# Kernel tuning notes

Hardware: AMD Instinct MI355X
Metric: run time of the kernel (lower is better)

Reference implementation:

```python
import jax, jax.numpy as jnp
import numpy as np

ATT, WEMB, VIEW, ADIM, EMB = 312, 512, 16, 2048, 2048
B = 2048
IN = ATT + WEMB + VIEW * WEMB  # 9016; output_dim defaults to input_dim
EPS = 1e-8  # torch cosine_similarity eps


def setup_inputs() -> dict:
    key = jax.random.key(0)
    ks = jax.random.split(key, 8)
    s = 0.02
    return {
        "x": jax.random.normal(ks[0], (B, IN), dtype=jnp.float32),
        "Wq": s * jax.random.normal(ks[1], (WEMB, ADIM), dtype=jnp.float32),
        "bq": jnp.zeros((ADIM,), jnp.float32),
        "Wk": s * jax.random.normal(ks[2], (WEMB, ADIM), dtype=jnp.float32),
        "bk": jnp.zeros((ADIM,), jnp.float32),
        "Wv": s * jax.random.normal(ks[3], (WEMB, ADIM), dtype=jnp.float32),
        "bv": jnp.zeros((ADIM,), jnp.float32),
        "Wm": s * jax.random.normal(ks[4], (ATT + ADIM, EMB), dtype=jnp.float32),
        "bm": jnp.zeros((EMB,), jnp.float32),
        "Wd1": s * jax.random.normal(ks[5], (EMB, 4096), dtype=jnp.float32),
        "bd1": jnp.zeros((4096,), jnp.float32),
        "Wd2": s * jax.random.normal(ks[6], (4096, IN), dtype=jnp.float32),
        "bd2": jnp.zeros((IN,), jnp.float32),
    }


def reference(x, Wq, bq, Wk, bk, Wv, bv, Wm, bm, Wd1, bd1, Wd2, bd2):
    att_emb = x[:, :ATT]                                   # [B, 312]
    desc_emb = x[:, ATT:ATT + WEMB]                        # [B, 512]
    gpt_emb = x[:, ATT + WEMB:].reshape(x.shape[0], -1, WEMB)  # [B, V, 512]

    # q is the same projected desc for every view (expand before linear)
    q = desc_emb @ Wq + bq                                 # [B, A]
    k = jnp.einsum("bvw,wa->bva", gpt_emb, Wk) + bk        # [B, V, A]
    v = jnp.einsum("bvw,wa->bva", gpt_emb, Wv) + bv        # [B, V, A]

    # cosed score: cosine similarity * L2 distance
    dot = jnp.einsum("bva,ba->bv", k, q)                   # [B, V]
    qn = jnp.maximum(jnp.linalg.norm(q, axis=-1), EPS)     # [B]
    kn = jnp.maximum(jnp.linalg.norm(k, axis=-1), EPS)     # [B, V]
    cs = dot / (qn[:, None] * kn)
    ed = jnp.linalg.norm(q[:, None, :] - k, axis=-1)       # [B, V]
    attn = jax.nn.softmax(cs * ed, axis=-1)                # [B, V]

    # torch.matmul([B,V], [B,V,A]) -> [B,B,A]; .mean(dim=1) averages over the
    # attn-batch axis, i.e. fused[j] = mean_b(attn[b]) @ v[j]. Compute the
    # mathematically identical form without the BxBxA intermediate.
    attn_mean = attn.mean(axis=0)                          # [V]
    fused = jnp.einsum("v,bva->ba", attn_mean, v)          # [B, A]

    z = jax.nn.relu(jnp.concatenate([att_emb, fused], axis=1) @ Wm + bm)  # [B, EMB]
    h = jax.nn.relu(z @ Wd1 + bd1)                          # [B, 4096]
    return h @ Wd2 + bd2                                    # [B, IN]
```

## Files before the change

### kernel.cpp

```cpp
#include <hip/hip_runtime.h>


typedef __bf16 bf16x8 __attribute__((ext_vector_type(8)));
typedef float  f32x4  __attribute__((ext_vector_type(4)));
typedef unsigned short u16;

#define ATT   312
#define WEMB  512
#define VIEW  16
#define ADIM  2048
#define EMB   2048
#define BATCH 2048
#define INDIM 9016
#define KCAT  2360
#define KCATP 2432
#define NOUT  9016
#define NOUTP 9216

__device__ __forceinline__ u16 f2bf(float f) {
  unsigned u = __builtin_bit_cast(unsigned, f);
  u += 0x7FFFu + ((u >> 16) & 1u);
  return (u16)(u >> 16);
}
__device__ __forceinline__ float bf2f(u16 b) {
  unsigned u = (unsigned)b << 16;
  return __builtin_bit_cast(float, u);
}

__device__ __forceinline__ void gl_lds16(const u16* g, u16* l) {
  __builtin_amdgcn_global_load_lds((const __attribute__((address_space(1))) void*)g,
                                   (__attribute__((address_space(3))) void*)l, 16, 0, 0);
}

__global__ void castx_k(const float* __restrict__ x, u16* __restrict__ cc,
                        u16* __restrict__ desc, u16* __restrict__ gpt) {
  const int b = blockIdx.x, t = threadIdx.x;
  const float4* row = (const float4*)(x + (size_t)b * INDIM);
  for (int c = t; c < INDIM / 4; c += 256) {
    float4 v = row[c];
    ushort4 o = make_ushort4(f2bf(v.x), f2bf(v.y), f2bf(v.z), f2bf(v.w));
    if (c < ATT / 4)                 *(ushort4*)&cc[(size_t)b * KCATP + c * 4] = o;
    else if (c < (ATT + WEMB) / 4)   *(ushort4*)&desc[(size_t)b * WEMB + (c - ATT / 4) * 4] = o;
    else                             *(ushort4*)&gpt[(size_t)b * (VIEW * WEMB) + (c - (ATT + WEMB) / 4) * 4] = o;
  }
  if (t < (KCATP - KCAT) / 4) {
    *(ushort4*)&cc[(size_t)b * KCATP + KCAT + t * 4] = make_ushort4(0, 0, 0, 0);
  }
}

struct TcDesc { const float* src; u16* dst; int K, N, Kp, Np, ntx, base; };
struct TcArgs { TcDesc d[6]; };

__global__ void transcast6_k(TcArgs A) {
  __shared__ float tile[64][65];
  int mi = 0;
  const int bid = blockIdx.x;
#pragma unroll
  for (int i = 1; i < 6; ++i) if (bid >= A.d[i].base) mi = i;
  const TcDesc& D = A.d[mi];
  const int local = bid - D.base;
  const int n0 = (local % D.ntx) * 64, k0 = (local / D.ntx) * 64;
  const int t = threadIdx.x;
  const int tr = t >> 4, tc4 = (t & 15) * 4;
#pragma unroll
  for (int i = 0; i < 4; ++i) {
    const int k = k0 + tr + i * 16;
    float v0 = 0.f, v1 = 0.f, v2 = 0.f, v3 = 0.f;
    if (k < D.K) {
      const int n = n0 + tc4;
      const float* p = D.src + (size_t)k * D.N + n;
      if (n + 3 < D.N) { float4 v = *(const float4*)p; v0 = v.x; v1 = v.y; v2 = v.z; v3 = v.w; }
      else {
        if (n + 0 < D.N) v0 = p[0];
        if (n + 1 < D.N) v1 = p[1];
        if (n + 2 < D.N) v2 = p[2];
        if (n + 3 < D.N) v3 = p[3];
      }
    }
    tile[tr + i * 16][tc4 + 0] = v0;
    tile[tr + i * 16][tc4 + 1] = v1;
    tile[tr + i * 16][tc4 + 2] = v2;
    tile[tr + i * 16][tc4 + 3] = v3;
  }
  __syncthreads();
#pragma unroll
  for (int i = 0; i < 4; ++i) {
    const int rn = tr + i * 16;
    const int n = n0 + rn;
    const int kk = k0 + tc4;
    if (n < D.Np && kk < D.Kp) {
      const bool nv = (n < D.N);
      ushort4 o = make_ushort4(f2bf(nv ? tile[tc4 + 0][rn] : 0.f),
                               f2bf(nv ? tile[tc4 + 1][rn] : 0.f),
                               f2bf(nv ? tile[tc4 + 2][rn] : 0.f),
                               f2bf(nv ? tile[tc4 + 3][rn] : 0.f));
      *(ushort4*)&D.dst[(size_t)n * D.Kp + kk] = o;
    }
  }
}

__device__ __forceinline__ void stage_half(const u16* __restrict__ src, int ld,
                                           u16* dst, int wave, int lane) {
#pragma unroll
  for (int j = 0; j < 2; ++j) {
    const int s = wave * 2 + j;
    const int r = ((s >> 1) << 4) + (lane >> 2);
    const int c = ((s & 1) << 5) +
                  (((lane & 3) << 3) ^ (((lane >> 5) & 1) << 4));
    gl_lds16(src + (long)r * ld + c, dst + s * 512 + (lane << 3));
  }
}

#define BAR   __builtin_amdgcn_s_barrier()
#define LGKM0 asm volatile("s_waitcnt lgkmcnt(0)" ::: "memory")
#define VM6   asm volatile("s_waitcnt vmcnt(6)" ::: "memory")
#define VM4   asm volatile("s_waitcnt vmcnt(4)" ::: "memory")
#define VM0   asm volatile("s_waitcnt vmcnt(0)" ::: "memory")

#define RDA(bufo, lo, hi) do { _Pragma("unroll") for (int mf = (lo); mf <= (hi); ++mf) \
  _Pragma("unroll") for (int kk = 0; kk < 2; ++kk) \
    a[mf][kk] = *(const bf16x8*)&lds[(bufo) + aoff0 + (mf * 2 + kk) * 512]; } while (0)
#define RDB(bufo, lo, hi) do { _Pragma("unroll") for (int nf = (lo); nf <= (hi); ++nf) \
  _Pragma("unroll") for (int kk = 0; kk < 2; ++kk) \
    b[nf][kk] = *(const bf16x8*)&lds[(bufo) + boff0 + nf * 1024 + kk * 512]; } while (0)
#define QUAD(qm, qn) do { __builtin_amdgcn_s_setprio(1); \
  _Pragma("unroll") for (int m4 = 0; m4 < 4; ++m4) \
  _Pragma("unroll") for (int n2 = 0; n2 < 2; ++n2) \
  _Pragma("unroll") for (int kk = 0; kk < 2; ++kk) \
    acc[(qm) * 4 + m4][(qn) * 2 + n2] = __builtin_amdgcn_mfma_f32_16x16x32_bf16( \
        a[(qm) * 4 + m4][kk], b[(qn) * 2 + n2][kk], acc[(qm) * 4 + m4][(qn) * 2 + n2], 0, 0, 0); \
  __builtin_amdgcn_s_setprio(0); } while (0)

template <int MODE>
__global__ __launch_bounds__(512, 2)
void gemm256(const u16* __restrict__ A, const u16* __restrict__ BT,
             const float* __restrict__ bias, int K, int Nreal,
             float* __restrict__ dstF, u16* __restrict__ dstH,
             float* __restrict__ PF, int ldc,
             const float* __restrict__ qbuf, float* __restrict__ dotb,
             float* __restrict__ kn2b, int mt, int nt, int fastm) {
  __shared__ alignas(16) u16 lds[65536];
  int tm, tn, ksl = 0, kloc = K;
  long koff = 0;
  if (MODE == 5) {
    if ((int)blockIdx.x < 256) {
      const int w = ((blockIdx.x & 7) << 5) + (blockIdx.x >> 3);
      tm = w & 7; tn = w >> 3;
    } else {
      const int b2 = blockIdx.x - 256;
      const int w = ((b2 & 7) << 5) + (b2 >> 3);
      const int tile = w >> 3; ksl = w & 7;
      tm = tile & 7; tn = 32 + (tile >> 3);
      kloc = 512; koff = (long)ksl * 512;
    }
  } else if (MODE == 6) {
    const int w = ((blockIdx.x & 7) << 5) + (blockIdx.x >> 3);
    ksl = w & 1;
    const int tile = w >> 1;
    tm = tile & 7; tn = tile >> 3;
    kloc = K >> 1; koff = (long)ksl * kloc;
  } else {
    const int nwg = mt * nt;
    const int xcd = blockIdx.x & 7, idx = blockIdx.x >> 3;
    const int qq = nwg >> 3, rr = nwg & 7;
    const int wg = (xcd < rr ? xcd * (qq + 1) : rr * (qq + 1) + (xcd - rr) * qq) + idx;
    if (fastm) { tm = wg % mt; tn = wg / mt; } else { tn = wg % nt; tm = wg / nt; }
  }

  const int tid = threadIdx.x;
  const int wave = tid >> 6, lane = tid & 63;
  const long m0 = (long)tm * 256, n0 = (long)tn * 256;
  const int wm = wave >> 2, wn = wave & 3;
  const u16* Ab = A + m0 * K + koff;
  const u16* Bb = BT + n0 * K + koff;

  f32x4 acc[8][4] = {};
  bf16x8 a[8][2], b[4][2];
  const int LP = (lane & 15) * 32 + ((((lane >> 4) << 3)) ^ (((lane >> 3) & 1) << 4));
  const int aoff0 = wm * 8192 + LP;
  const int boff0 = 16384 + (wn >> 1) * 8192 + (wn & 1) * 4096 + LP;
  const int NT = kloc >> 6;

  stage_half(Ab,                K, &lds[0],     wave, lane);
  stage_half(Ab + 128 * K,      K, &lds[8192],  wave, lane);
  stage_half(Bb,                K, &lds[16384], wave, lane);
  stage_half(Bb + 128 * K,      K, &lds[24576], wave, lane);
  stage_half(Ab + 64,           K, &lds[32768], wave, lane);
  stage_half(Ab + 128 * K + 64, K, &lds[40960], wave, lane);
  stage_half(Bb + 64,           K, &lds[49152], wave, lane);
  VM6; BAR;

  const int iters = NT >> 1;
  for (int i = 0; i < iters; ++i) {
    const int t0 = 2 * i;
    const bool nl = (i < iters - 1);
    RDA(0, 0, 3); RDB(0, 0, 1);
    stage_half(Bb + 128 * K + (t0 + 1) * 64, K, &lds[57344], wave, lane);
    BAR; LGKM0; QUAD(0, 0); BAR;
    RDA(0, 4, 7);
    BAR; LGKM0; QUAD(1, 0); BAR;
    RDB(0, 2, 3);
    if (nl) stage_half(Ab + (t0 + 2) * 64, K, &lds[0], wave, lane);
    BAR; LGKM0; QUAD(0, 1); BAR;
    if (nl) stage_half(Ab + 128 * K + (t0 + 2) * 64, K, &lds[8192], wave, lane);
    BAR; QUAD(1, 1);
    if (nl) { VM4; } else { VM0; }
    BAR;
    RDA(32768, 0, 3); RDB(32768, 0, 1);
    if (nl) stage_half(Bb + (t0 + 2) * 64, K, &lds[16384], wave, lane);
    BAR; LGKM0; QUAD(0, 0); BAR;
    RDA(32768, 4, 7);
    if (nl) stage_half(Bb + 128 * K + (t0 + 2) * 64, K, &lds[24576], wave, lane);
    BAR; LGKM0; QUAD(1, 0); BAR;
    RDB(32768, 2, 3);
    if (nl) stage_half(Ab + (t0 + 3) * 64, K, &lds[32768], wave, lane);
    BAR; LGKM0; QUAD(0, 1); BAR;
    if (nl) {
      stage_half(Ab + 128 * K + (t0 + 3) * 64, K, &lds[40960], wave, lane);
      stage_half(Bb + (t0 + 3) * 64, K, &lds[49152], wave, lane);
    }
    BAR; QUAD(1, 1);
    if (nl) VM6;
    BAR;
  }

  const int lr = lane >> 4, lc = lane & 15;
  if (MODE == 2) {
#pragma unroll
    for (int mf = 0; mf < 8; ++mf) {
#pragma unroll
      for (int r = 0; r < 4; ++r) {
        const long grow = m0 + wm * 128 + mf * 16 + lr * 4 + r;
        const long bb = grow >> 4;
        float ds = 0.f, ks2 = 0.f;
#pragma unroll
        for (int nf = 0; nf < 4; ++nf) {
          const long col = n0 + wn * 64 + nf * 16 + lc;
          float kv = acc[mf][nf][r] + bias[col];
          ds += kv * qbuf[bb * ADIM + col];
          ks2 += kv * kv;
        }
#pragma unroll
        for (int m = 1; m < 16; m <<= 1) {
          ds += __shfl_xor(ds, m, 64);
          ks2 += __shfl_xor(ks2, m, 64);
        }
        if (lc == 0) {
          atomicAdd(&dotb[grow], ds);
          atomicAdd(&kn2b[grow], ks2);
        }
      }
    }
  } else if (MODE == 5) {
    if (ksl == 0) {
#pragma unroll
      for (int mf = 0; mf < 8; ++mf) {
#pragma unroll
        for (int nf = 0; nf < 4; ++nf) {
          const long col = n0 + wn * 64 + nf * 16 + lc;
          if (col < Nreal) {
            const float bv_ = bias[col];
#pragma unroll
            for (int r = 0; r < 4; ++r) {
              const long row = m0 + wm * 128 + mf * 16 + lr * 4 + r;
              dstF[row * (long)ldc + col] = acc[mf][nf][r] + bv_;
            }
          }
        }
      }
    } else {
      float* pt = PF + (long)(ksl - 1) * BATCH * 1024;
#pragma unroll
      for (int mf = 0; mf < 8; ++mf) {
#pragma unroll
        for (int nf = 0; nf < 4; ++nf) {
          const long col = n0 + wn * 64 + nf * 16 + lc;
#pragma unroll
          for (int r = 0; r < 4; ++r) {
            const long row = m0 + wm * 128 + mf * 16 + lr * 4 + r;
            pt[row * 1024 + (col - 8192)] = acc[mf][nf][r];
          }
        }
      }
    }
  } else {
#pragma unroll
    for (int mf = 0; mf < 8; ++mf) {
#pragma unroll
      for (int nf = 0; nf < 4; ++nf) {
        const long col = n0 + wn * 64 + nf * 16 + lc;
        const float bv_ = bias[col];
#pragma unroll
        for (int r = 0; r < 4; ++r) {
          const long row = m0 + wm * 128 + mf * 16 + lr * 4 + r;
          if (ksl == 0) dstH[row * (long)ldc + col] = f2bf(acc[mf][nf][r] + bv_);
          else          PF[row * (long)ldc + col] = acc[mf][nf][r];
        }
      }
    }
  }
}

__global__ void relucast2_k(u16* __restrict__ h, const float* __restrict__ ph) {
  const size_t i = ((size_t)blockIdx.x * 256 + threadIdx.x) * 8;
  bf16x8 hv = *(const bf16x8*)&h[i];
  float4 pa = *(const float4*)&ph[i];
  float4 pb = *(const float4*)&ph[i + 4];
  ushort4 o0 = make_ushort4(f2bf(fmaxf((float)hv[0] + pa.x, 0.f)),
                            f2bf(fmaxf((float)hv[1] + pa.y, 0.f)),
                            f2bf(fmaxf((float)hv[2] + pa.z, 0.f)),
                            f2bf(fmaxf((float)hv[3] + pa.w, 0.f)));
  ushort4 o1 = make_ushort4(f2bf(fmaxf((float)hv[4] + pb.x, 0.f)),
                            f2bf(fmaxf((float)hv[5] + pb.y, 0.f)),
                            f2bf(fmaxf((float)hv[6] + pb.z, 0.f)),
                            f2bf(fmaxf((float)hv[7] + pb.w, 0.f)));
  *(ushort4*)&h[i] = o0;
  *(ushort4*)&h[i + 4] = o1;
}

__global__ void tailred_k(float* __restrict__ out, const float* __restrict__ pt) {
  const int i = blockIdx.x * 256 + threadIdx.x;
  const int row = i / 206, c = (i % 206) * 4;
  float4 acc = *(float4*)&out[(size_t)row * NOUT + 8192 + c];
#pragma unroll
  for (int s = 0; s < 7; ++s) {
    float4 p = *(const float4*)&pt[(size_t)s * BATCH * 1024 + (size_t)row * 1024 + c];
    acc.x += p.x; acc.y += p.y; acc.z += p.z; acc.w += p.w;
  }
  *(float4*)&out[(size_t)row * NOUT + 8192 + c] = acc;
}

template <int MODE, bool RELU>
__global__ __launch_bounds__(256, 2)
void gemm_bt(const u16* __restrict__ A, const u16* __restrict__ BT,
             const float* __restrict__ bias, int K, int Nreal,
             float* __restrict__ dstF, u16* __restrict__ dstH, int ldc,
             int mt, int nt, int fastm) {
  __shared__ alignas(16) u16 Ash[128 * 64];
  __shared__ alignas(16) u16 Bsh[128 * 64];
  const int nwg = mt * nt;
  const int xcd = blockIdx.x & 7, idx = blockIdx.x >> 3;
  const int qq = nwg >> 3, rr = nwg & 7;
  const int wg = (xcd < rr ? xcd * (qq + 1) : rr * (qq + 1) + (xcd - rr) * qq) + idx;
  int tm, tn;
  if (fastm) { tm = wg % mt; tn = wg / mt; } else { tn = wg % nt; tm = wg / nt; }

  const int tid = threadIdx.x;
  const int wave = tid >> 6, lane = tid & 63;
  const long m0 = (long)tm * 128;
  const long n0 = (long)tn * 128;
  const int wm = wave >> 1, wnn = wave & 1;
  f32x4 acc[4][4] = {};

  const int srow = (wave << 5) + (lane >> 3);
  const int scol = (lane & 7) << 3;

  for (int k0 = 0; k0 < K; k0 += 64) {
    __syncthreads();
#pragma unroll
    for (int i = 0; i < 4; ++i) {
      const int r = srow + i * 8;
      gl_lds16(A + (m0 + r) * (long)K + k0 + scol, &Ash[r * 64 + scol]);
      gl_lds16(BT + (n0 + r) * (long)K + k0 + scol, &Bsh[r * 64 + scol]);
    }
    __syncthreads();
#pragma unroll
    for (int kb = 0; kb < 2; ++kb) {
      bf16x8 af[4], bfv[4];
#pragma unroll
      for (int f = 0; f < 4; ++f) {
        af[f]  = *(const bf16x8*)&Ash[(wm * 64 + f * 16 + (lane & 15)) * 64 + kb * 32 + (lane >> 4) * 8];
        bfv[f] = *(const bf16x8*)&Bsh[(wnn * 64 + f * 16 + (lane & 15)) * 64 + kb * 32 + (lane >> 4) * 8];
      }
#pragma unroll
      for (int mf = 0; mf < 4; ++mf)
#pragma unroll
        for (int nf = 0; nf < 4; ++nf)
          acc[mf][nf] = __builtin_amdgcn_mfma_f32_16x16x32_bf16(af[mf], bfv[nf], acc[mf][nf], 0, 0, 0);
    }
  }

  const int lr = lane >> 4, lc = lane & 15;
#pragma unroll
  for (int mf = 0; mf < 4; ++mf) {
#pragma unroll
    for (int nf = 0; nf < 4; ++nf) {
      const long col = n0 + wnn * 64 + nf * 16 + lc;
      if (col < Nreal) {
        const float bv_ = bias[col];
#pragma unroll
        for (int r = 0; r < 4; ++r) {
          const long row = m0 + wm * 64 + mf * 16 + lr * 4 + r;
          float v = acc[mf][nf][r] + bv_;
          if (RELU) v = fmaxf(v, 0.f);
          if (MODE == 0) dstF[row * (long)ldc + col] = v;
          else           dstH[row * (long)ldc + col] = f2bf(v);
        }
      }
    }
  }
}

__global__ void qnorm_k(const float* __restrict__ q, float* __restrict__ qn2) {
  const int b = blockIdx.x, t = threadIdx.x;
  const float4* row = (const float4*)(q + (size_t)b * ADIM);
  float s = 0.f;
#pragma unroll
  for (int i = 0; i < 2; ++i) {
    float4 v = row[t + i * 256];
    s += v.x * v.x + v.y * v.y + v.z * v.z + v.w * v.w;
  }
#pragma unroll
  for (int m = 1; m < 64; m <<= 1) s += __shfl_xor(s, m, 64);
  __shared__ float wsum[4];
  if ((t & 63) == 0) wsum[t >> 6] = s;
  __syncthreads();
  if (t == 0) qn2[b] = wsum[0] + wsum[1] + wsum[2] + wsum[3];
}

__global__ void attn_k(const float* __restrict__ dotb, const float* __restrict__ kn2b,
                       const float* __restrict__ qn2, float* __restrict__ asum) {
  const int b = blockIdx.x * 256 + threadIdx.x;
  const int lane = threadIdx.x & 63;
  const float q2 = qn2[b];
  const float qn = fmaxf(sqrtf(q2), 1e-8f);
  float lg[VIEW];
  float mx = -1e30f;
#pragma unroll
  for (int v = 0; v < VIEW; ++v) {
    const float d = dotb[b * VIEW + v], k2 = kn2b[b * VIEW + v];
    const float kn = fmaxf(sqrtf(k2), 1e-8f);
    const float cs = d / (qn * kn);
    const float ed = sqrtf(fmaxf(q2 - 2.f * d + k2, 0.f));
    lg[v] = cs * ed;
    mx = fmaxf(mx, lg[v]);
  }
  float s = 0.f;
#pragma unroll
  for (int v = 0; v < VIEW; ++v) { lg[v] = expf(lg[v] - mx); s += lg[v]; }
  const float inv = 1.f / s;
#pragma unroll
  for (int v = 0; v < VIEW; ++v) {
    float aa = lg[v] * inv;
#pragma unroll
    for (int m = 1; m < 64; m <<= 1) aa += __shfl_xor(aa, m, 64);
    if (lane == 0) atomicAdd(&asum[v], aa);
  }
}

__global__ void gtilde_k(const u16* __restrict__ gpt, const float* __restrict__ asum,
                         u16* __restrict__ g) {
  const int b = blockIdx.x, t = threadIdx.x;
  float am[VIEW];
#pragma unroll
  for (int v = 0; v < VIEW; ++v) am[v] = asum[v] * (1.f / (float)BATCH);
  float s[8] = {};
  const u16* gx = gpt + (size_t)b * (VIEW * WEMB) + t * 8;
#pragma unroll
  for (int v = 0; v < VIEW; ++v) {
    bf16x8 gv = *(const bf16x8*)&gx[v * WEMB];
#pragma unroll
    for (int j = 0; j < 8; ++j) s[j] += am[v] * (float)gv[j];
  }
  ushort4 o0, o1;
  o0 = make_ushort4(f2bf(s[0]), f2bf(s[1]), f2bf(s[2]), f2bf(s[3]));
  o1 = make_ushort4(f2bf(s[4]), f2bf(s[5]), f2bf(s[6]), f2bf(s[7]));
  *(ushort4*)&g[(size_t)b * WEMB + t * 8] = o0;
  *(ushort4*)&g[(size_t)b * WEMB + t * 8 + 4] = o1;
}

extern "C" void kernel_launch(void* const* d_in, const int* in_sizes, int n_in,
                              void* d_out, int out_size, void* d_ws, size_t ws_size,
                              hipStream_t stream) {
  const float* x   = (const float*)d_in[0];
  const float* Wq  = (const float*)d_in[1];
  const float* bq  = (const float*)d_in[2];
  const float* Wk  = (const float*)d_in[3];
  const float* bk  = (const float*)d_in[4];
  const float* Wv  = (const float*)d_in[5];
  const float* bv  = (const float*)d_in[6];
  const float* Wm  = (const float*)d_in[7];
  const float* bm  = (const float*)d_in[8];
  const float* Wd1 = (const float*)d_in[9];
  const float* bd1 = (const float*)d_in[10];
  const float* Wd2 = (const float*)d_in[11];
  const float* bd2 = (const float*)d_in[12];
  float* out = (float*)d_out;

  char* ws = (char*)d_ws;
  size_t off = 0;
  auto alloc = [&](size_t bytes) -> void* {
    void* p = ws + off;
    off = (off + bytes + 255) & ~(size_t)255;
    return p;
  };
  u16* WqT  = (u16*)alloc((size_t)ADIM * WEMB * 2);
  u16* WkT  = (u16*)alloc((size_t)ADIM * WEMB * 2);
  u16* WvT  = (u16*)alloc((size_t)ADIM * WEMB * 2);
  u16* WmT  = (u16*)alloc((size_t)EMB * KCATP * 2);
  u16* Wd1T = (u16*)alloc((size_t)4096 * EMB * 2);
  u16* Wd2T = (u16*)alloc((size_t)NOUTP * 4096 * 2);
  u16* desc = (u16*)alloc((size_t)BATCH * WEMB * 2);
  u16* gpt  = (u16*)alloc((size_t)BATCH * VIEW * WEMB * 2);
  u16* cc   = (u16*)alloc((size_t)BATCH * KCATP * 2);
  float* q    = (float*)alloc((size_t)BATCH * ADIM * 4);
  float* qn2  = (float*)alloc((size_t)BATCH * 4);
  float* stats = (float*)alloc((size_t)(BATCH * VIEW * 2 + 64) * 4);
  float* dotb = stats;
  float* kn2b = stats + BATCH * VIEW;
  float* asum = stats + BATCH * VIEW * 2;
  u16* gt = (u16*)alloc((size_t)BATCH * WEMB * 2);
  u16* z  = (u16*)alloc((size_t)BATCH * EMB * 2);
  u16* h  = (u16*)alloc((size_t)BATCH * 4096 * 2);
  if (off > ws_size) return;
  float* Ph    = (float*)desc;
  float* Ptail = (float*)desc;

  hipMemsetAsync(stats, 0, (size_t)(BATCH * VIEW * 2 + 64) * 4, stream);

  castx_k<<<BATCH, 256, 0, stream>>>(x, cc, desc, gpt);

  TcArgs ta;
  int base = 0;
  auto setd = [&](int i, const float* s, u16* d, int K, int N, int Kp, int Np) {
    ta.d[i] = TcDesc{s, d, K, N, Kp, Np, (Np + 63) / 64, base};
    base += ((Np + 63) / 64) * ((Kp + 63) / 64);
  };
  setd(0, Wq, WqT, WEMB, ADIM, WEMB, ADIM);
  setd(1, Wk, WkT, WEMB, ADIM, WEMB, ADIM);
  setd(2, Wv, WvT, WEMB, ADIM, WEMB, ADIM);
  setd(3, Wm, WmT, KCAT, EMB, KCATP, EMB);
  setd(4, Wd1, Wd1T, EMB, 4096, EMB, 4096);
  setd(5, Wd2, Wd2T, 4096, NOUT, 4096, NOUTP);
  transcast6_k<<<base, 256, 0, stream>>>(ta);

  gemm_bt<0, false><<<16 * 16, 256, 0, stream>>>(
      desc, WqT, bq, WEMB, ADIM, q, nullptr, ADIM, BATCH / 128, ADIM / 128, 0);
  qnorm_k<<<BATCH, 256, 0, stream>>>(q, qn2);
  gemm256<2><<<128 * 8, 512, 0, stream>>>(
      gpt, WkT, bk, WEMB, ADIM, nullptr, nullptr, nullptr, 0, q, dotb, kn2b,
      BATCH * VIEW / 256, ADIM / 256, 0);
  attn_k<<<BATCH / 256, 256, 0, stream>>>(dotb, kn2b, qn2, asum);
  gtilde_k<<<BATCH, 64, 0, stream>>>(gpt, asum, gt);
  gemm_bt<1, false><<<16 * 16, 256, 0, stream>>>(
      gt, WvT, bv, WEMB, ADIM, nullptr, cc + ATT, KCATP, BATCH / 128, ADIM / 128, 0);
  gemm_bt<1, true><<<16 * 16, 256, 0, stream>>>(
      cc, WmT, bm, KCATP, EMB, nullptr, z, EMB, BATCH / 128, EMB / 128, 0);
  gemm256<6><<<256, 512, 0, stream>>>(
      z, Wd1T, bd1, EMB, 4096, nullptr, h, Ph, 4096, nullptr, nullptr, nullptr,
      0, 0, 0);
  relucast2_k<<<(BATCH * 4096) / 2048, 256, 0, stream>>>(h, Ph);
  gemm256<5><<<512, 512, 0, stream>>>(
      h, Wd2T, bd2, 4096, NOUT, out, nullptr, Ptail, NOUT, nullptr, nullptr, nullptr,
      0, 0, 0);
  tailred_k<<<(BATCH * 206 * 4) / 1024, 256, 0, stream>>>(out, Ptail);
}
```

Before: 658.4 us.

## Run Wd2 GEMM as one persistent wave and fuse q-norm into q GEMM

```diff
diff --git a/kernel.cpp b/kernel.cpp
--- a/kernel.cpp
+++ b/kernel.cpp
@@ -15,16 +15,11 @@
 #define KCAT  2360
 #define KCATP 2432
 #define NOUT  9016
-#define NOUTP 9216
 
 __device__ __forceinline__ u16 f2bf(float f) {
   unsigned u = __builtin_bit_cast(unsigned, f);
   u += 0x7FFFu + ((u >> 16) & 1u);
   return (u16)(u >> 16);
-}
-__device__ __forceinline__ float bf2f(u16 b) {
-  unsigned u = (unsigned)b << 16;
-  return __builtin_bit_cast(float, u);
 }
 
 __device__ __forceinline__ void gl_lds16(const u16* g, u16* l) {
@@ -131,56 +126,13 @@
         a[(qm) * 4 + m4][kk], b[(qn) * 2 + n2][kk], acc[(qm) * 4 + m4][(qn) * 2 + n2], 0, 0, 0); \
   __builtin_amdgcn_s_setprio(0); } while (0)
 
-template <int MODE>
-__global__ __launch_bounds__(512, 2)
-void gemm256(const u16* __restrict__ A, const u16* __restrict__ BT,
-             const float* __restrict__ bias, int K, int Nreal,
-             float* __restrict__ dstF, u16* __restrict__ dstH,
-             float* __restrict__ PF, int ldc,
-             const float* __restrict__ qbuf, float* __restrict__ dotb,
-             float* __restrict__ kn2b, int mt, int nt, int fastm) {
-  __shared__ alignas(16) u16 lds[65536];
-  int tm, tn, ksl = 0, kloc = K;
-  long koff = 0;
-  if (MODE == 5) {
-    if ((int)blockIdx.x < 256) {
-      const int w = ((blockIdx.x & 7) << 5) + (blockIdx.x >> 3);
-      tm = w & 7; tn = w >> 3;
-    } else {
-      const int b2 = blockIdx.x - 256;
-      const int w = ((b2 & 7) << 5) + (b2 >> 3);
-      const int tile = w >> 3; ksl = w & 7;
-      tm = tile & 7; tn = 32 + (tile >> 3);
-      kloc = 512; koff = (long)ksl * 512;
-    }
-  } else if (MODE == 6) {
-    const int w = ((blockIdx.x & 7) << 5) + (blockIdx.x >> 3);
-    ksl = w & 1;
-    const int tile = w >> 1;
-    tm = tile & 7; tn = tile >> 3;
-    kloc = K >> 1; koff = (long)ksl * kloc;
-  } else {
-    const int nwg = mt * nt;
-    const int xcd = blockIdx.x & 7, idx = blockIdx.x >> 3;
-    const int qq = nwg >> 3, rr = nwg & 7;
-    const int wg = (xcd < rr ? xcd * (qq + 1) : rr * (qq + 1) + (xcd - rr) * qq) + idx;
-    if (fastm) { tm = wg % mt; tn = wg / mt; } else { tn = wg % nt; tm = wg / nt; }
-  }
-
-  const int tid = threadIdx.x;
-  const int wave = tid >> 6, lane = tid & 63;
-  const long m0 = (long)tm * 256, n0 = (long)tn * 256;
-  const int wm = wave >> 2, wn = wave & 3;
-  const u16* Ab = A + m0 * K + koff;
-  const u16* Bb = BT + n0 * K + koff;
-
-  f32x4 acc[8][4] = {};
+__device__ __forceinline__ void gemm_core(const u16* __restrict__ Ab,
+                                          const u16* __restrict__ Bb,
+                                          int K, int kloc, u16* lds,
+                                          f32x4 (&acc)[8][4],
+                                          int aoff0, int boff0,
+                                          int wave, int lane) {
   bf16x8 a[8][2], b[4][2];
-  const int LP = (lane & 15) * 32 + ((((lane >> 4) << 3)) ^ (((lane >> 3) & 1) << 4));
-  const int aoff0 = wm * 8192 + LP;
-  const int boff0 = 16384 + (wn >> 1) * 8192 + (wn & 1) * 4096 + LP;
-  const int NT = kloc >> 6;
-
   stage_half(Ab,                K, &lds[0],     wave, lane);
   stage_half(Ab + 128 * K,      K, &lds[8192],  wave, lane);
   stage_half(Bb,                K, &lds[16384], wave, lane);
@@ -190,7 +142,7 @@
   stage_half(Bb + 64,           K, &lds[49152], wave, lane);
   VM6; BAR;
 
-  const int iters = NT >> 1;
+  const int iters = (kloc >> 6) >> 1;
   for (int i = 0; i < iters; ++i) {
     const int t0 = 2 * i;
     const bool nl = (i < iters - 1);
@@ -223,8 +175,108 @@
     if (nl) VM6;
     BAR;
   }
-
+}
+
+template <int MODE>
+__global__ __launch_bounds__(512, 2)
+void gemm256(const u16* __restrict__ A, const u16* __restrict__ BT,
+             const float* __restrict__ bias, int K, int Nreal,
+             float* __restrict__ dstF, u16* __restrict__ dstH,
+             float* __restrict__ PF, int ldc,
+             const float* __restrict__ qbuf, float* __restrict__ dotb,
+             float* __restrict__ kn2b, int mt, int nt, int fastm) {
+  __shared__ alignas(16) u16 lds[65536];
+  const int tid = threadIdx.x;
+  const int wave = tid >> 6, lane = tid & 63;
+  const int wm = wave >> 2, wn = wave & 3;
+  const int LP = (lane & 15) * 32 + ((((lane >> 4) << 3)) ^ (((lane >> 3) & 1) << 4));
+  const int aoff0 = wm * 8192 + LP;
+  const int boff0 = 16384 + (wn >> 1) * 8192 + (wn & 1) * 4096 + LP;
   const int lr = lane >> 4, lc = lane & 15;
+
+  f32x4 acc[8][4] = {};
+
+  if (MODE == 8) {
+    const int w = ((blockIdx.x & 7) << 5) + (blockIdx.x >> 3);
+    const int tm = w & 7, tn = w >> 3;
+    const long m0 = (long)tm * 256, n0 = (long)tn * 256;
+    gemm_core(A + m0 * K, BT + n0 * K, K, K, lds, acc, aoff0, boff0, wave, lane);
+#pragma unroll
+    for (int mf = 0; mf < 8; ++mf) {
+#pragma unroll
+      for (int nf = 0; nf < 4; ++nf) {
+        const long col = n0 + wn * 64 + nf * 16 + lc;
+        const float bv_ = bias[col];
+#pragma unroll
+        for (int r = 0; r < 4; ++r) {
+          const long row = m0 + wm * 128 + mf * 16 + lr * 4 + r;
+          dstF[row * (long)ldc + col] = acc[mf][nf][r] + bv_;
+        }
+      }
+    }
+    const int tile = blockIdx.x >> 3, ksl = blockIdx.x & 7;
+    const int tm2 = tile & 7, tn2 = 32 + (tile >> 3);
+    const long m2 = (long)tm2 * 256, n2 = (long)tn2 * 256;
+    const long koff = (long)ksl * 512;
+#pragma unroll
+    for (int mf = 0; mf < 8; ++mf)
+#pragma unroll
+      for (int nf = 0; nf < 4; ++nf) acc[mf][nf] = (f32x4){0.f, 0.f, 0.f, 0.f};
+    gemm_core(A + m2 * K + koff, BT + n2 * K + koff, K, 512, lds, acc,
+              aoff0, boff0, wave, lane);
+    if (ksl == 0) {
+#pragma unroll
+      for (int mf = 0; mf < 8; ++mf) {
+#pragma unroll
+        for (int nf = 0; nf < 4; ++nf) {
+          const long col = n2 + wn * 64 + nf * 16 + lc;
+          if (col < Nreal) {
+            const float bv_ = bias[col];
+#pragma unroll
+            for (int r = 0; r < 4; ++r) {
+              const long row = m2 + wm * 128 + mf * 16 + lr * 4 + r;
+              dstF[row * (long)ldc + col] = acc[mf][nf][r] + bv_;
+            }
+          }
+        }
+      }
+    } else {
+      float* pt = PF + (long)(ksl - 1) * BATCH * 1024;
+#pragma unroll
+      for (int mf = 0; mf < 8; ++mf) {
+#pragma unroll
+        for (int nf = 0; nf < 4; ++nf) {
+          const long col = n2 + wn * 64 + nf * 16 + lc;
+#pragma unroll
+          for (int r = 0; r < 4; ++r) {
+            const long row = m2 + wm * 128 + mf * 16 + lr * 4 + r;
+            pt[row * 1024 + (col - 8192)] = acc[mf][nf][r];
+          }
+        }
+      }
+    }
+    return;
+  }
+
+  int tm, tn, ksl = 0, kloc = K;
+  long koff = 0;
+  if (MODE == 6) {
+    const int w = ((blockIdx.x & 7) << 5) + (blockIdx.x >> 3);
+    ksl = w & 1;
+    const int tile = w >> 1;
+    tm = tile & 7; tn = tile >> 3;
+    kloc = K >> 1; koff = (long)ksl * kloc;
+  } else {
+    const int nwg = mt * nt;
+    const int xcd = blockIdx.x & 7, idx = blockIdx.x >> 3;
+    const int qq = nwg >> 3, rr = nwg & 7;
+    const int wg = (xcd < rr ? xcd * (qq + 1) : rr * (qq + 1) + (xcd - rr) * qq) + idx;
+    if (fastm) { tm = wg % mt; tn = wg / mt; } else { tn = wg % nt; tm = wg / nt; }
+  }
+  const long m0 = (long)tm * 256, n0 = (long)tn * 256;
+  gemm_core(A + m0 * K + koff, BT + n0 * K + koff, K, kloc, lds, acc,
+            aoff0, boff0, wave, lane);
+
   if (MODE == 2) {
 #pragma unroll
     for (int mf = 0; mf < 8; ++mf) {
@@ -248,38 +300,6 @@
         if (lc == 0) {
           atomicAdd(&dotb[grow], ds);
           atomicAdd(&kn2b[grow], ks2);
-        }
-      }
-    }
-  } else if (MODE == 5) {
-    if (ksl == 0) {
-#pragma unroll
-      for (int mf = 0; mf < 8; ++mf) {
-#pragma unroll
-        for (int nf = 0; nf < 4; ++nf) {
-          const long col = n0 + wn * 64 + nf * 16 + lc;
-          if (col < Nreal) {
-            const float bv_ = bias[col];
-#pragma unroll
-            for (int r = 0; r < 4; ++r) {
-              const long row = m0 + wm * 128 + mf * 16 + lr * 4 + r;
-              dstF[row * (long)ldc + col] = acc[mf][nf][r] + bv_;
-            }
-          }
-        }
-      }
-    } else {
-      float* pt = PF + (long)(ksl - 1) * BATCH * 1024;
-#pragma unroll
-      for (int mf = 0; mf < 8; ++mf) {
-#pragma unroll
-        for (int nf = 0; nf < 4; ++nf) {
-          const long col = n0 + wn * 64 + nf * 16 + lc;
-#pragma unroll
-          for (int r = 0; r < 4; ++r) {
-            const long row = m0 + wm * 128 + mf * 16 + lr * 4 + r;
-            pt[row * 1024 + (col - 8192)] = acc[mf][nf][r];
-          }
         }
       }
     }
@@ -335,7 +355,7 @@
 void gemm_bt(const u16* __restrict__ A, const u16* __restrict__ BT,
              const float* __restrict__ bias, int K, int Nreal,
              float* __restrict__ dstF, u16* __restrict__ dstH, int ldc,
-             int mt, int nt, int fastm) {
+             float* __restrict__ qn2buf, int mt, int nt, int fastm) {
   __shared__ alignas(16) u16 Ash[128 * 64];
   __shared__ alignas(16) u16 Bsh[128 * 64];
   const int nwg = mt * nt;
@@ -383,6 +403,7 @@
   const int lr = lane >> 4, lc = lane & 15;
 #pragma unroll
   for (int mf = 0; mf < 4; ++mf) {
+    float rs[4] = {0.f, 0.f, 0.f, 0.f};
 #pragma unroll
     for (int nf = 0; nf < 4; ++nf) {
       const long col = n0 + wnn * 64 + nf * 16 + lc;
@@ -393,29 +414,25 @@
           const long row = m0 + wm * 64 + mf * 16 + lr * 4 + r;
           float v = acc[mf][nf][r] + bv_;
           if (RELU) v = fmaxf(v, 0.f);
-          if (MODE == 0) dstF[row * (long)ldc + col] = v;
-          else           dstH[row * (long)ldc + col] = f2bf(v);
-        }
-      }
-    }
-  }
-}
-
-__global__ void qnorm_k(const float* __restrict__ q, float* __restrict__ qn2) {
-  const int b = blockIdx.x, t = threadIdx.x;
-  const float4* row = (const float4*)(q + (size_t)b * ADIM);
-  float s = 0.f;
-#pragma unroll
-  for (int i = 0; i < 2; ++i) {
-    float4 v = row[t + i * 256];
-    s += v.x * v.x + v.y * v.y + v.z * v.z + v.w * v.w;
-  }
-#pragma unroll
-  for (int m = 1; m < 64; m <<= 1) s += __shfl_xor(s, m, 64);
-  __shared__ float wsum[4];
-  if ((t & 63) == 0) wsum[t >> 6] = s;
-  __syncthreads();
-  if (t == 0) qn2[b] = wsum[0] + wsum[1] + wsum[2] + wsum[3];
+          if (MODE == 0 || MODE == 7) dstF[row * (long)ldc + col] = v;
+          else                        dstH[row * (long)ldc + col] = f2bf(v);
+          if (MODE == 7) rs[r] += v * v;
+        }
+      }
+    }
+    if (MODE == 7) {
+#pragma unroll
+      for (int r = 0; r < 4; ++r) {
+        float s = rs[r];
+#pragma unroll
+        for (int m = 1; m < 16; m <<= 1) s += __shfl_xor(s, m, 64);
+        if (lc == 0) {
+          const long row = m0 + wm * 64 + mf * 16 + lr * 4 + r;
+          atomicAdd(&qn2buf[row], s);
+        }
+      }
+    }
+  }
 }
 
 __global__ void attn_k(const float* __restrict__ dotb, const float* __restrict__ kn2b,
@@ -499,16 +516,16 @@
   u16* WvT  = (u16*)alloc((size_t)ADIM * WEMB * 2);
   u16* WmT  = (u16*)alloc((size_t)EMB * KCATP * 2);
   u16* Wd1T = (u16*)alloc((size_t)4096 * EMB * 2);
-  u16* Wd2T = (u16*)alloc((size_t)NOUTP * 4096 * 2);
+  u16* Wd2T = (u16*)alloc((size_t)(9216) * 4096 * 2);
   u16* desc = (u16*)alloc((size_t)BATCH * WEMB * 2);
   u16* gpt  = (u16*)alloc((size_t)BATCH * VIEW * WEMB * 2);
   u16* cc   = (u16*)alloc((size_t)BATCH * KCATP * 2);
   float* q    = (float*)alloc((size_t)BATCH * ADIM * 4);
-  float* qn2  = (float*)alloc((size_t)BATCH * 4);
-  float* stats = (float*)alloc((size_t)(BATCH * VIEW * 2 + 64) * 4);
+  float* stats = (float*)alloc((size_t)(BATCH * VIEW * 2 + 64 + BATCH) * 4);
   float* dotb = stats;
   float* kn2b = stats + BATCH * VIEW;
   float* asum = stats + BATCH * VIEW * 2;
+  float* qn2  = stats + BATCH * VIEW * 2 + 64;
   u16* gt = (u16*)alloc((size_t)BATCH * WEMB * 2);
   u16* z  = (u16*)alloc((size_t)BATCH * EMB * 2);
   u16* h  = (u16*)alloc((size_t)BATCH * 4096 * 2);
@@ -516,7 +533,7 @@
   float* Ph    = (float*)desc;
   float* Ptail = (float*)desc;
 
-  hipMemsetAsync(stats, 0, (size_t)(BATCH * VIEW * 2 + 64) * 4, stream);
+  hipMemsetAsync(stats, 0, (size_t)(BATCH * VIEW * 2 + 64 + BATCH) * 4, stream);
 
   castx_k<<<BATCH, 256, 0, stream>>>(x, cc, desc, gpt);
 
@@ -531,26 +548,25 @@
   setd(2, Wv, WvT, WEMB, ADIM, WEMB, ADIM);
   setd(3, Wm, WmT, KCAT, EMB, KCATP, EMB);
   setd(4, Wd1, Wd1T, EMB, 4096, EMB, 4096);
-  setd(5, Wd2, Wd2T, 4096, NOUT, 4096, NOUTP);
+  setd(5, Wd2, Wd2T, 4096, NOUT, 4096, 9216);
   transcast6_k<<<base, 256, 0, stream>>>(ta);
 
-  gemm_bt<0, false><<<16 * 16, 256, 0, stream>>>(
-      desc, WqT, bq, WEMB, ADIM, q, nullptr, ADIM, BATCH / 128, ADIM / 128, 0);
-  qnorm_k<<<BATCH, 256, 0, stream>>>(q, qn2);
+  gemm_bt<7, false><<<16 * 16, 256, 0, stream>>>(
+      desc, WqT, bq, WEMB, ADIM, q, nullptr, ADIM, qn2, BATCH / 128, ADIM / 128, 0);
   gemm256<2><<<128 * 8, 512, 0, stream>>>(
       gpt, WkT, bk, WEMB, ADIM, nullptr, nullptr, nullptr, 0, q, dotb, kn2b,
       BATCH * VIEW / 256, ADIM / 256, 0);
   attn_k<<<BATCH / 256, 256, 0, stream>>>(dotb, kn2b, qn2, asum);
   gtilde_k<<<BATCH, 64, 0, stream>>>(gpt, asum, gt);
   gemm_bt<1, false><<<16 * 16, 256, 0, stream>>>(
-      gt, WvT, bv, WEMB, ADIM, nullptr, cc + ATT, KCATP, BATCH / 128, ADIM / 128, 0);
+      gt, WvT, bv, WEMB, ADIM, nullptr, cc + ATT, KCATP, nullptr, BATCH / 128, ADIM / 128, 0);
   gemm_bt<1, true><<<16 * 16, 256, 0, stream>>>(
-      cc, WmT, bm, KCATP, EMB, nullptr, z, EMB, BATCH / 128, EMB / 128, 0);
+      cc, WmT, bm, KCATP, EMB, nullptr, z, EMB, nullptr, BATCH / 128, EMB / 128, 0);
   gemm256<6><<<256, 512, 0, stream>>>(
       z, Wd1T, bd1, EMB, 4096, nullptr, h, Ph, 4096, nullptr, nullptr, nullptr,
       0, 0, 0);
   relucast2_k<<<(BATCH * 4096) / 2048, 256, 0, stream>>>(h, Ph);
-  gemm256<5><<<512, 512, 0, stream>>>(
+  gemm256<8><<<256, 512, 0, stream>>>(
       h, Wd2T, bd2, 4096, NOUT, out, nullptr, Ptail, NOUT, nullptr, nullptr, nullptr,
       0, 0, 0);
   tailred_k<<<(BATCH * 206 * 4) / 1024, 256, 0, stream>>>(out, Ptail);
```

Measured after the change: 676.2 us. 2.7% more time.
